# Kernel optimization log

Hardware: AMD Instinct MI355X
Metric: run time of the kernel (lower is better)

Reference implementation:

```python
import jax, jax.numpy as jnp
import numpy as np

B_, L, DM = 2, 1024, 1024
D_STATE, D_CONV, EXPAND = 16, 4, 2
DI = EXPAND * DM          # 2048 inner dim
DTR = DM // 16            # 64 dt rank


def setup_inputs() -> dict:
    key = jax.random.key(0)
    ks = jax.random.split(key, 16)
    g = lambda k, shp, s: jax.random.normal(k, shp, jnp.float32) * s
    inp = {
        "x": g(ks[0], (B_, L, DM), 1.0),
        "ln_g": jnp.ones((DM,), jnp.float32),
        "ln_b": jnp.zeros((DM,), jnp.float32),
        "in_proj_w": g(ks[1], (2 * DI, DM), (2.0 / (DM + 2 * DI)) ** 0.5),
        "conv_w": g(ks[2], (DI, 1, D_CONV), (2.0 / D_CONV) ** 0.5),
        "conv_b": jnp.zeros((DI,), jnp.float32),
        "dtin_w": g(ks[3], (DTR, DI), (2.0 / (DI + DTR)) ** 0.5),
        "dtin_b": jnp.zeros((DTR,), jnp.float32),
        "dt_w": g(ks[4], (DI, DTR), DTR ** -0.5),
        "dt_b": jnp.log(jnp.expm1(jax.random.uniform(ks[5], (DI,), jnp.float32, 1e-3, 0.1))),  # inverse-softplus of dt in [dt_min, dt_max]
        "B_w": g(ks[6], (D_STATE, DI), DI ** -0.5),
        "C_w": g(ks[7], (D_STATE, DI), DI ** -0.5),
        "A_log": jnp.log(jnp.broadcast_to(jnp.arange(1, D_STATE + 1, dtype=jnp.float32), (DI, D_STATE))),
        "D": jnp.ones((DI,), jnp.float32),
        "out_w": g(ks[8], (DM, DI), (2.0 / (DM + DI)) ** 0.5),
    }
    return inp


def _layernorm(x, g, b, eps=1e-5):
    mu = jnp.mean(x, -1, keepdims=True)
    var = jnp.mean(jnp.square(x - mu), -1, keepdims=True)
    return (x - mu) * jax.lax.rsqrt(var + eps) * g + b


def _selective_scan(u, dt, Bm, Cm, A, Dp):
    # u,dt: (b,l,di); Bm,Cm: (b,l,n); A: (di,n)
    def step(h, inp):
        dt_t, B_t, C_t, u_t = inp  # (b,di),(b,n),(b,n),(b,di)
        dA = jnp.exp(dt_t[..., None] * A)                       # (b,di,n)
        h = h * dA + (dt_t * u_t)[..., None] * B_t[:, None, :]   # (b,di,n)
        y = jnp.einsum("bdn,bn->bd", h, C_t)
        return h, y

    tm = lambda a: jnp.swapaxes(a, 0, 1)  # time-major
    h0 = jnp.zeros((u.shape[0], u.shape[2], A.shape[1]), u.dtype)
    _, ys = jax.lax.scan(step, h0, (tm(dt), tm(Bm), tm(Cm), tm(u)))
    return jnp.swapaxes(ys, 0, 1) + u * Dp  # (b,l,di)


def reference(x, ln_g, ln_b, in_proj_w, conv_w, conv_b, dtin_w, dtin_b,
              dt_w, dt_b, B_w, C_w, A_log, D, out_w):
    residual = x
    xn = _layernorm(x, ln_g, ln_b)
    xz = xn @ in_proj_w.T                       # (b,l,2*di)
    x_proj, z = jnp.split(xz, 2, axis=-1)
    # causal depthwise conv1d (left pad d_conv-1, truncate to seq_len)
    xp = jnp.pad(x_proj, ((0, 0), (D_CONV - 1, 0), (0, 0)))
    x_conv = conv_b
    for k in range(D_CONV):
        x_conv = x_conv + conv_w[:, 0, k] * xp[:, k:k + L, :]
    x_conv = jax.nn.silu(x_conv)
    dt_in = x_conv @ dtin_w.T + dtin_b          # (b,l,dtr)
    dt = jax.nn.softplus(dt_in @ dt_w.T + dt_b) # (b,l,di)
    Bm = x_conv @ B_w.T                         # (b,l,n)
    Cm = x_conv @ C_w.T
    A = -jnp.exp(A_log)                         # (di,n)
    y = _selective_scan(x_conv, dt, Bm, Cm, A, D)
    y = y * jax.nn.silu(z)
    return y @ out_w.T + residual
```

## Files before the change

### kernel.cpp

```cpp
#include <hip/hip_runtime.h>
#include <hip/hip_bf16.h>
#include <cstdint>

#define BL    2
#define LSEQ  1024
#define DMOD  1024
#define DIN   2048
#define NST   16
#define DTRK  64
#define MR    (BL*LSEQ)

#define CCH 32
#define TCH 32
#define KSPLIT 8

typedef __bf16 bf16x8 __attribute__((ext_vector_type(8)));
typedef float  f32x4  __attribute__((ext_vector_type(4)));

#if __has_builtin(__builtin_amdgcn_exp2f)
#define EXP2F(x) __builtin_amdgcn_exp2f(x)
#else
#define EXP2F(x) exp2f(x)
#endif
#define LOG2E 1.4426950408889634f

__device__ __forceinline__ void glds16(const void* g, const void* l) {
    __builtin_amdgcn_global_load_lds(
        (__attribute__((address_space(1))) void*)(uintptr_t)(g),
        (__attribute__((address_space(3))) void*)(uint32_t)(uintptr_t)(l),
        16, 0, 0);
}

template <int MODE, int TM, int TN>
__global__ __launch_bounds__(256, 4) void gemm_bt(
    const __hip_bfloat16* __restrict__ A, int lda,
    const __hip_bfloat16* __restrict__ Bw, int ldb,
    int M, int N, int Ksl,
    void* __restrict__ e0, void* __restrict__ e1,
    const float* __restrict__ bias)
{
    constexpr int WM = TM / 2, WN = TN / 2;
    constexpr int MT = WM / 16, NT = WN / 16;
    constexpr int NDA = TM / 64, NDB = TN / 64;
    __shared__ __align__(16) __hip_bfloat16 sA[2][TM * 32];
    __shared__ __align__(16) __hip_bfloat16 sB[2][TN * 32];

    int bx = blockIdx.x, by = blockIdx.y;
    if ((gridDim.y & 7) == 0) {
        const int bid = blockIdx.x + gridDim.x * blockIdx.y;
        const int xcd = bid & 7, s = bid >> 3;
        bx = s % gridDim.x;
        by = (s / gridDim.x) * 8 + xcd;
    }
    const int m0 = by * TM;
    const int n0 = bx * TN;
    const int k0 = blockIdx.z * Ksl;
    const int tid = threadIdx.x;
    const int w = tid >> 6, lane = tid & 63;
    const int wm = (w >> 1) * WM, wn = (w & 1) * WN;
    const int lrow = lane & 15, lq = lane >> 4;

    const int r0 = tid >> 2;
    const int qs = ((tid & 3) - (r0 >> 1)) & 3;
    const __hip_bfloat16* pa[NDA];
    const __hip_bfloat16* pb[NDB];
#pragma unroll
    for (int i = 0; i < NDA; i++) pa[i] = A + (size_t)(m0 + r0 + 64 * i) * lda + k0 + qs * 8;
#pragma unroll
    for (int i = 0; i < NDB; i++) pb[i] = Bw + (size_t)(n0 + r0 + 64 * i) * ldb + k0 + qs * 8;

    f32x4 acc[MT][NT];
#pragma unroll
    for (int i = 0; i < MT; i++)
#pragma unroll
        for (int j = 0; j < NT; j++) { acc[i][j][0]=0.f; acc[i][j][1]=0.f; acc[i][j][2]=0.f; acc[i][j][3]=0.f; }

    const int nk = Ksl >> 5;
#pragma unroll
    for (int i = 0; i < NDA; i++) glds16(pa[i], &sA[0][i * 2048 + tid * 8]);
#pragma unroll
    for (int i = 0; i < NDB; i++) glds16(pb[i], &sB[0][i * 2048 + tid * 8]);

    for (int kb = 0; kb < nk; ++kb) {
        const int cur = kb & 1, nxt = cur ^ 1;
        __syncthreads();
        if (kb + 1 < nk) {
#pragma unroll
            for (int i = 0; i < NDA; i++) { pa[i] += 32; glds16(pa[i], &sA[nxt][i * 2048 + tid * 8]); }
#pragma unroll
            for (int i = 0; i < NDB; i++) { pb[i] += 32; glds16(pb[i], &sB[nxt][i * 2048 + tid * 8]); }
        }
        bf16x8 af[MT], bb[NT];
#pragma unroll
        for (int mt = 0; mt < MT; mt++) {
            const int row = wm + mt * 16 + lrow;
            af[mt] = *(const bf16x8*)&sA[cur][row * 32 + (((lq + (row >> 1)) & 3) * 8)];
        }
#pragma unroll
        for (int nt = 0; nt < NT; nt++) {
            const int row = wn + nt * 16 + lrow;
            bb[nt] = *(const bf16x8*)&sB[cur][row * 32 + (((lq + (row >> 1)) & 3) * 8)];
        }
#pragma unroll
        for (int mt = 0; mt < MT; mt++)
#pragma unroll
            for (int nt = 0; nt < NT; nt++)
                acc[mt][nt] = __builtin_amdgcn_mfma_f32_16x16x32_bf16(af[mt], bb[nt], acc[mt][nt], 0, 0, 0);
    }

#pragma unroll
    for (int mt = 0; mt < MT; mt++) {
#pragma unroll
        for (int nt = 0; nt < NT; nt++) {
            const int gn = n0 + wn + nt * 16 + lrow;
            if (gn >= N) continue;
            const int gmb = m0 + wm + mt * 16 + lq * 4;
#pragma unroll
            for (int r = 0; r < 4; r++) {
                const int gm = gmb + r;
                const float v = acc[mt][nt][r];
                if (MODE == 0) {
                    if (gn < DIN) ((__hip_bfloat16*)e0)[(size_t)gm * DIN + gn] = __float2bfloat16(v);
                    else {
                        const float s = v / (1.f + __expf(-v));
                        ((__hip_bfloat16*)e1)[(size_t)gm * DIN + (gn - DIN)] = __float2bfloat16(s);
                    }
                } else if (MODE == 1) {
                    ((float*)e0)[((size_t)blockIdx.z * M + gm) * 96 + gn] = v;
                } else if (MODE == 2) {
                    const float xx = v + bias[gn];
                    ((float*)e0)[(size_t)gm * N + gn] = (xx > 20.f) ? xx : log1pf(__expf(xx));
                } else {
                    ((float*)e0)[(size_t)gm * N + gn] = v + ((const float*)e1)[(size_t)gm * N + gn];
                }
            }
        }
    }
}

__global__ void ep1_kernel(const float* __restrict__ part, const float* __restrict__ dtin_b,
                           __hip_bfloat16* __restrict__ dtinb, float* __restrict__ Bmf,
                           float* __restrict__ Cmf) {
    const int i = blockIdx.x * 256 + threadIdx.x;
    if (i >= MR * 96) return;
    const int m = i / 96, n = i - m * 96;
    float s = 0.f;
#pragma unroll
    for (int z = 0; z < KSPLIT; z++) s += part[((size_t)z * MR + m) * 96 + n];
    if (n < 64)      dtinb[(size_t)m * 64 + n] = __float2bfloat16(s + dtin_b[n]);
    else if (n < 80) Bmf[(size_t)m * NST + (n - 64)] = s;
    else             Cmf[(size_t)m * NST + (n - 80)] = s;
}

__global__ void cvt_all(const float* __restrict__ w_in, const float* __restrict__ dtin_w,
                        const float* __restrict__ B_w, const float* __restrict__ C_w,
                        const float* __restrict__ dt_w, const float* __restrict__ out_w,
                        __hip_bfloat16* __restrict__ w1b, __hip_bfloat16* __restrict__ wpb,
                        __hip_bfloat16* __restrict__ dtwb, __hip_bfloat16* __restrict__ owb) {
    const int NV = (4194304 + 131072 + 32768 + 32768 + 131072 + 2097152) / 4;
    for (int v = blockIdx.x * 256 + threadIdx.x; v < NV; v += gridDim.x * 256) {
        const int i = v * 4;
        const float* s; __hip_bfloat16* dk;
        if      (i < 4194304) { s = w_in   + i;             dk = w1b  + i; }
        else if (i < 4325376) { s = dtin_w + (i - 4194304); dk = wpb  + (i - 4194304); }
        else if (i < 4358144) { s = B_w    + (i - 4325376); dk = wpb  + 131072 + (i - 4325376); }
        else if (i < 4390912) { s = C_w    + (i - 4358144); dk = wpb  + 163840 + (i - 4358144); }
        else if (i < 4521984) { s = dt_w   + (i - 4390912); dk = dtwb + (i - 4390912); }
        else                  { s = out_w  + (i - 4521984); dk = owb  + (i - 4521984); }
        const float4 f = *(const float4*)s;
        __hip_bfloat16 t0 = __float2bfloat16(f.x), t1 = __float2bfloat16(f.y);
        __hip_bfloat16 t2 = __float2bfloat16(f.z), t3 = __float2bfloat16(f.w);
        ushort4 o;
        o.x = *(unsigned short*)&t0; o.y = *(unsigned short*)&t1;
        o.z = *(unsigned short*)&t2; o.w = *(unsigned short*)&t3;
        *(ushort4*)dk = o;
    }
}

__global__ void ln_kernel(const float* __restrict__ x, const float* __restrict__ g,
                          const float* __restrict__ b, __hip_bfloat16* __restrict__ xn) {
    const int row = blockIdx.x;
    const int tid = threadIdx.x;
    const float4 v = ((const float4*)(x + (size_t)row * DMOD))[tid];
    float s  = v.x + v.y + v.z + v.w;
    float sq = v.x * v.x + v.y * v.y + v.z * v.z + v.w * v.w;
#pragma unroll
    for (int off = 32; off >= 1; off >>= 1) {
        s  += __shfl_down(s, off, 64);
        sq += __shfl_down(sq, off, 64);
    }
    __shared__ float red[8];
    const int w = tid >> 6, lane = tid & 63;
    if (lane == 0) { red[w] = s; red[4 + w] = sq; }
    __syncthreads();
    s  = red[0] + red[1] + red[2] + red[3];
    sq = red[4] + red[5] + red[6] + red[7];
    const float mean = s * (1.f / DMOD);
    const float rstd = rsqrtf(sq * (1.f / DMOD) - mean * mean + 1e-5f);
    const int col = tid * 4;
    const float vv[4] = {v.x, v.y, v.z, v.w};
#pragma unroll
    for (int i = 0; i < 4; i++)
        xn[(size_t)row * DMOD + col + i] =
            __float2bfloat16((vv[i] - mean) * rstd * g[col + i] + b[col + i]);
}

__global__ void conv_silu_kernel(const __hip_bfloat16* __restrict__ xp, const float* __restrict__ cw,
                                 const float* __restrict__ cb,
                                 __hip_bfloat16* __restrict__ xcb) {
    const int d = blockIdx.x * 256 + threadIdx.x;
    const int m0 = blockIdx.y * 64;
    const int l0 = m0 & (LSEQ - 1);
    const float w0 = cw[d * 4], w1 = cw[d * 4 + 1], w2 = cw[d * 4 + 2], w3 = cw[d * 4 + 3];
    const float cbd = cb[d];
    float x0 = 0.f, x1 = 0.f, x2 = 0.f;
    if (l0 != 0) {
        x0 = __bfloat162float(xp[(size_t)(m0 - 3) * DIN + d]);
        x1 = __bfloat162float(xp[(size_t)(m0 - 2) * DIN + d]);
        x2 = __bfloat162float(xp[(size_t)(m0 - 1) * DIN + d]);
    }
#pragma unroll 4
    for (int i = 0; i < 64; i++) {
        const float x3 = __bfloat162float(xp[(size_t)(m0 + i) * DIN + d]);
        const float a = cbd + w0 * x0 + w1 * x1 + w2 * x2 + w3 * x3;
        const float sv = a / (1.f + __expf(-a));
        xcb[(size_t)(m0 + i) * DIN + d] = __float2bfloat16(sv);
        x0 = x1; x1 = x2; x2 = x3;
    }
}


__global__ __launch_bounds__(256) void scan_p1(
    const float* __restrict__ dt, const __hip_bfloat16* __restrict__ u,
    const float* __restrict__ Bm, const float* __restrict__ A_log,
    float* __restrict__ Aprod, float* __restrict__ Bacc)
{
    __shared__ float sB[TCH * NST];
    const int blk = blockIdx.x;
    const int bb = blk >> 9, c = (blk >> 4) & 31, dtile = blk & 15;
    const int tid = threadIdx.x;
    const int nh = tid & 1, dl = tid >> 1;
    const int d = dtile * 128 + dl;
    const int row0 = bb * LSEQ + c * TCH;

    sB[tid]       = Bm[(size_t)row0 * NST + tid];
    sB[tid + 256] = Bm[(size_t)row0 * NST + tid + 256];
    __syncthreads();

    float a2[8];
    {
        const float4 al0 = *(const float4*)&A_log[(size_t)d * NST + nh * 8];
        const float4 al1 = *(const float4*)&A_log[(size_t)d * NST + nh * 8 + 4];
        a2[0] = -__expf(al0.x) * LOG2E; a2[1] = -__expf(al0.y) * LOG2E;
        a2[2] = -__expf(al0.z) * LOG2E; a2[3] = -__expf(al0.w) * LOG2E;
        a2[4] = -__expf(al1.x) * LOG2E; a2[5] = -__expf(al1.y) * LOG2E;
        a2[6] = -__expf(al1.z) * LOG2E; a2[7] = -__expf(al1.w) * LOG2E;
    }
    const float* pdt = dt + (size_t)row0 * DIN + d;
    const __hip_bfloat16* pu = u + (size_t)row0 * DIN + d;
    float h[8], Ap[8];
#pragma unroll
    for (int j = 0; j < 8; j++) { h[j] = 0.f; Ap[j] = 1.f; }

#pragma unroll 4
    for (int t = 0; t < TCH; t++) {
        const float dtv = pdt[t * DIN];
        const float uv  = __bfloat162float(pu[t * DIN]);
        const float du = dtv * uv;
        float bv[8];
        *(float4*)&bv[0] = *(const float4*)&sB[t * NST + nh * 8];
        *(float4*)&bv[4] = *(const float4*)&sB[t * NST + nh * 8 + 4];
#pragma unroll
        for (int j = 0; j < 8; j++) {
            const float e = EXP2F(dtv * a2[j]);
            Ap[j] *= e;
            h[j] = h[j] * e + du * bv[j];
        }
    }
    const size_t idx = (((size_t)bb * CCH + c) * DIN + d) * NST + nh * 8;
    *(float4*)&Aprod[idx]     = make_float4(Ap[0], Ap[1], Ap[2], Ap[3]);
    *(float4*)&Aprod[idx + 4] = make_float4(Ap[4], Ap[5], Ap[6], Ap[7]);
    *(float4*)&Bacc[idx]      = make_float4(h[0], h[1], h[2], h[3]);
    *(float4*)&Bacc[idx + 4]  = make_float4(h[4], h[5], h[6], h[7]);
}

__global__ __launch_bounds__(256) void scan_p2(
    const float* __restrict__ Aprod, const float* __restrict__ Bacc,
    float* __restrict__ hstart)
{
    const int i = blockIdx.x * 256 + threadIdx.x;
    const int bb = i >> 15;
    const int dn = i & 32767;
    float hs = 0.f;
#pragma unroll
    for (int c = 0; c < CCH; c++) {
        const size_t idx = (((size_t)bb * CCH + c) << 15) + dn;
        hstart[idx] = hs;
        hs = Aprod[idx] * hs + Bacc[idx];
    }
}

__global__ __launch_bounds__(256) void scan_p3(
    const float* __restrict__ dt, const __hip_bfloat16* __restrict__ u,
    const float* __restrict__ Bm, const float* __restrict__ Cm,
    const float* __restrict__ A_log, const float* __restrict__ Dp,
    const __hip_bfloat16* __restrict__ zs, const float* __restrict__ hstart,
    __hip_bfloat16* __restrict__ y)
{
    __shared__ float sB[TCH * NST], sC[TCH * NST];
    const int blk = blockIdx.x;
    const int bb = blk >> 9, c = (blk >> 4) & 31, dtile = blk & 15;
    const int tid = threadIdx.x;
    const int nh = tid & 1, dl = tid >> 1;
    const int d = dtile * 128 + dl;
    const int row0 = bb * LSEQ + c * TCH;

    sB[tid]       = Bm[(size_t)row0 * NST + tid];
    sB[tid + 256] = Bm[(size_t)row0 * NST + tid + 256];
    sC[tid]       = Cm[(size_t)row0 * NST + tid];
    sC[tid + 256] = Cm[(size_t)row0 * NST + tid + 256];
    __syncthreads();

    float a2[8];
    {
        const float4 al0 = *(const float4*)&A_log[(size_t)d * NST + nh * 8];
        const float4 al1 = *(const float4*)&A_log[(size_t)d * NST + nh * 8 + 4];
        a2[0] = -__expf(al0.x) * LOG2E; a2[1] = -__expf(al0.y) * LOG2E;
        a2[2] = -__expf(al0.z) * LOG2E; a2[3] = -__expf(al0.w) * LOG2E;
        a2[4] = -__expf(al1.x) * LOG2E; a2[5] = -__expf(al1.y) * LOG2E;
        a2[6] = -__expf(al1.z) * LOG2E; a2[7] = -__expf(al1.w) * LOG2E;
    }
    const float Dd = Dp[d];
    const size_t idx = (((size_t)bb * CCH + c) * DIN + d) * NST + nh * 8;
    float h[8];
    *(float4*)&h[0] = *(const float4*)&hstart[idx];
    *(float4*)&h[4] = *(const float4*)&hstart[idx + 4];

    const float* pdt = dt + (size_t)row0 * DIN + d;
    const __hip_bfloat16* pu = u + (size_t)row0 * DIN + d;
    const __hip_bfloat16* pz = zs + (size_t)row0 * DIN + d;
    __hip_bfloat16* py = y + (size_t)row0 * DIN + d;

#pragma unroll 2
    for (int t = 0; t < TCH; t++) {
        const float dtv = pdt[t * DIN];
        const float uv  = __bfloat162float(pu[t * DIN]);
        const float du = dtv * uv;
        float bv[8], cv[8];
        *(float4*)&bv[0] = *(const float4*)&sB[t * NST + nh * 8];
        *(float4*)&bv[4] = *(const float4*)&sB[t * NST + nh * 8 + 4];
        *(float4*)&cv[0] = *(const float4*)&sC[t * NST + nh * 8];
        *(float4*)&cv[4] = *(const float4*)&sC[t * NST + nh * 8 + 4];
        float yp = 0.f;
#pragma unroll
        for (int j = 0; j < 8; j++) {
            const float e = EXP2F(dtv * a2[j]);
            h[j] = h[j] * e + du * bv[j];
            yp += h[j] * cv[j];
        }
        yp += __shfl_xor(yp, 1, 64);
        if (nh == 0) {
            const float zv = __bfloat162float(pz[t * DIN]);
            py[t * DIN] = __float2bfloat16((yp + uv * Dd) * zv);
        }
    }
}

extern "C" void kernel_launch(void* const* d_in, const int* in_sizes, int n_in,
                              void* d_out, int out_size, void* d_ws, size_t ws_size,
                              hipStream_t stream) {
    const float* x      = (const float*)d_in[0];
    const float* ln_g   = (const float*)d_in[1];
    const float* ln_b   = (const float*)d_in[2];
    const float* w_in   = (const float*)d_in[3];
    const float* conv_w = (const float*)d_in[4];
    const float* conv_b = (const float*)d_in[5];
    const float* dtin_w = (const float*)d_in[6];
    const float* dtin_b = (const float*)d_in[7];
    const float* dt_w   = (const float*)d_in[8];
    const float* dt_b   = (const float*)d_in[9];
    const float* B_w    = (const float*)d_in[10];
    const float* C_w    = (const float*)d_in[11];
    const float* A_log  = (const float*)d_in[12];
    const float* Dp     = (const float*)d_in[13];
    const float* out_w  = (const float*)d_in[14];
    float* out = (float*)d_out;

    char* ws = (char*)d_ws;
    auto alloc = [&](size_t bytes) { char* p = ws; ws += (bytes + 255) & ~255ull; return p; };
    __hip_bfloat16* w1b   = (__hip_bfloat16*)alloc((size_t)4096 * 1024 * 2);
    __hip_bfloat16* wpb   = (__hip_bfloat16*)alloc((size_t)96 * 2048 * 2);
    __hip_bfloat16* dtwb  = (__hip_bfloat16*)alloc((size_t)2048 * 64 * 2);
    __hip_bfloat16* owb   = (__hip_bfloat16*)alloc((size_t)1024 * 2048 * 2);
    __hip_bfloat16* xnb   = (__hip_bfloat16*)alloc((size_t)MR * DMOD * 2);
    __hip_bfloat16* xprojb= (__hip_bfloat16*)alloc((size_t)MR * DIN * 2);
    __hip_bfloat16* zs    = (__hip_bfloat16*)alloc((size_t)MR * DIN * 2);
    __hip_bfloat16* xcb   = (__hip_bfloat16*)alloc((size_t)MR * DIN * 2);
    __hip_bfloat16* dtinb = (__hip_bfloat16*)alloc((size_t)MR * 64 * 2);
    float*          Bmf   = (float*)alloc((size_t)MR * NST * 4);
    float*          Cmf   = (float*)alloc((size_t)MR * NST * 4);
    float*          dtf   = (float*)alloc((size_t)MR * DIN * 4);
    __hip_bfloat16* yb    = (__hip_bfloat16*)alloc((size_t)MR * DIN * 2);
    float*          Aprod = (float*)alloc((size_t)BL * CCH * DIN * NST * 4);
    float*          Bacc  = (float*)alloc((size_t)BL * CCH * DIN * NST * 4);
    float*          hstart= (float*)alloc((size_t)BL * CCH * DIN * NST * 4);
    float*          part  = (float*)w1b;

    cvt_all<<<1024, 256, 0, stream>>>(w_in, dtin_w, B_w, C_w, dt_w, out_w, w1b, wpb, dtwb, owb);
    ln_kernel<<<MR, 256, 0, stream>>>(x, ln_g, ln_b, xnb);

    gemm_bt<0, 64, 128><<<dim3(32, 32, 1), 256, 0, stream>>>(xnb, 1024, w1b, 1024, MR, 4096, 1024,
                                                             xprojb, zs, nullptr);
    conv_silu_kernel<<<dim3(8, 32), 256, 0, stream>>>(xprojb, conv_w, conv_b, xcb);

    gemm_bt<1, 64, 128><<<dim3(1, 32, KSPLIT), 256, 0, stream>>>(xcb, 2048, wpb, 2048, MR, 96, 2048 / KSPLIT,
                                                                 part, nullptr, nullptr);
    ep1_kernel<<<(MR * 96 + 255) / 256, 256, 0, stream>>>(part, dtin_b, dtinb, Bmf, Cmf);

    gemm_bt<2, 64, 128><<<dim3(16, 32, 1), 256, 0, stream>>>(dtinb, 64, dtwb, 64, MR, DIN, 64,
                                                             dtf, nullptr, dt_b);

    scan_p1<<<BL * CCH * 16, 256, 0, stream>>>(dtf, xcb, Bmf, A_log, Aprod, Bacc);
    scan_p2<<<BL * DIN * NST / 256, 256, 0, stream>>>(Aprod, Bacc, hstart);
    scan_p3<<<BL * CCH * 16, 256, 0, stream>>>(dtf, xcb, Bmf, Cmf, A_log, Dp, zs, hstart, yb);

    gemm_bt<3, 64, 64><<<dim3(16, 32, 1), 256, 0, stream>>>(yb, 2048, owb, 2048, MR, DMOD, 2048,
                                                            out, (void*)x, nullptr);
}
```

Baseline: 253.9 us.

## Fuse prep kernels, use atomic split-K, bf16 dt, and merge scan phases

Merges weight conversion, layernorm, zeroing of accumulators, and the residual copy into one prep kernel. The x_proj GEMM now reduces its split-K partials with atomics, which removes the epilogue kernel. The dt GEMM adds the bias and converts to bf16 while staging its A tile, and writes dt as bf16 to halve scan traffic. Scan phases 1 and 2 are merged using a last-block counter, and the out-projection uses 128x128 tiles with 4-way split-K atomics onto the prefilled residual. In exchange it adds atomic contention, nondeterministic summation order, and reduced dt precision.

Measured after the change: 415.3 us. 63.6% more time.

```diff
diff --git a/kernel.cpp b/kernel.cpp
--- a/kernel.cpp
+++ b/kernel.cpp
@@ -12,7 +12,6 @@
 
 #define CCH 32
 #define TCH 32
-#define KSPLIT 8
 
 typedef __bf16 bf16x8 __attribute__((ext_vector_type(8)));
 typedef float  f32x4  __attribute__((ext_vector_type(4)));
@@ -31,13 +30,35 @@
         16, 0, 0);
 }
 
+__device__ __forceinline__ __bf16 f2b(float f) {
+    __hip_bfloat16 t = __float2bfloat16(f);
+    return *(__bf16*)&t;
+}
+
+__device__ __forceinline__ void stage_dtin(const float* __restrict__ Af,
+                                           const float* __restrict__ bias,
+                                           __hip_bfloat16* dst, int m0, int r0,
+                                           int qs, int kb) {
+    const int col0 = kb * 32 + qs * 8;
+    const float4 f0 = *(const float4*)&Af[(size_t)(m0 + r0) * 64 + col0];
+    const float4 f1 = *(const float4*)&Af[(size_t)(m0 + r0) * 64 + col0 + 4];
+    const float4 b0 = *(const float4*)&bias[col0];
+    const float4 b1 = *(const float4*)&bias[col0 + 4];
+    bf16x8 o;
+    o[0] = f2b(f0.x + b0.x); o[1] = f2b(f0.y + b0.y);
+    o[2] = f2b(f0.z + b0.z); o[3] = f2b(f0.w + b0.w);
+    o[4] = f2b(f1.x + b1.x); o[5] = f2b(f1.y + b1.y);
+    o[6] = f2b(f1.z + b1.z); o[7] = f2b(f1.w + b1.w);
+    *(bf16x8*)dst = o;
+}
+
 template <int MODE, int TM, int TN>
-__global__ __launch_bounds__(256, 4) void gemm_bt(
+__global__ __launch_bounds__(256, (TM * TN <= 8192) ? 4 : 2) void gemm_bt(
     const __hip_bfloat16* __restrict__ A, int lda,
     const __hip_bfloat16* __restrict__ Bw, int ldb,
     int M, int N, int Ksl,
-    void* __restrict__ e0, void* __restrict__ e1,
-    const float* __restrict__ bias)
+    void* __restrict__ e0, void* __restrict__ e1, void* __restrict__ e2,
+    const float* __restrict__ bias, const float* __restrict__ Af)
 {
     constexpr int WM = TM / 2, WN = TN / 2;
     constexpr int MT = WM / 16, NT = WN / 16;
@@ -64,8 +85,10 @@
     const int qs = ((tid & 3) - (r0 >> 1)) & 3;
     const __hip_bfloat16* pa[NDA];
     const __hip_bfloat16* pb[NDB];
-#pragma unroll
-    for (int i = 0; i < NDA; i++) pa[i] = A + (size_t)(m0 + r0 + 64 * i) * lda + k0 + qs * 8;
+    if constexpr (MODE != 2) {
+#pragma unroll
+        for (int i = 0; i < NDA; i++) pa[i] = A + (size_t)(m0 + r0 + 64 * i) * lda + k0 + qs * 8;
+    }
 #pragma unroll
     for (int i = 0; i < NDB; i++) pb[i] = Bw + (size_t)(n0 + r0 + 64 * i) * ldb + k0 + qs * 8;
 
@@ -76,8 +99,12 @@
         for (int j = 0; j < NT; j++) { acc[i][j][0]=0.f; acc[i][j][1]=0.f; acc[i][j][2]=0.f; acc[i][j][3]=0.f; }
 
     const int nk = Ksl >> 5;
-#pragma unroll
-    for (int i = 0; i < NDA; i++) glds16(pa[i], &sA[0][i * 2048 + tid * 8]);
+    if constexpr (MODE == 2) {
+        stage_dtin(Af, bias, &sA[0][tid * 8], m0, r0, qs, 0);
+    } else {
+#pragma unroll
+        for (int i = 0; i < NDA; i++) glds16(pa[i], &sA[0][i * 2048 + tid * 8]);
+    }
 #pragma unroll
     for (int i = 0; i < NDB; i++) glds16(pb[i], &sB[0][i * 2048 + tid * 8]);
 
@@ -85,8 +112,12 @@
         const int cur = kb & 1, nxt = cur ^ 1;
         __syncthreads();
         if (kb + 1 < nk) {
-#pragma unroll
-            for (int i = 0; i < NDA; i++) { pa[i] += 32; glds16(pa[i], &sA[nxt][i * 2048 + tid * 8]); }
+            if constexpr (MODE == 2) {
+                stage_dtin(Af, bias, &sA[nxt][tid * 8], m0, r0, qs, kb + 1);
+            } else {
+#pragma unroll
+                for (int i = 0; i < NDA; i++) { pa[i] += 32; glds16(pa[i], &sA[nxt][i * 2048 + tid * 8]); }
+            }
 #pragma unroll
             for (int i = 0; i < NDB; i++) { pb[i] += 32; glds16(pb[i], &sB[nxt][i * 2048 + tid * 8]); }
         }
@@ -126,83 +157,87 @@
                         ((__hip_bfloat16*)e1)[(size_t)gm * DIN + (gn - DIN)] = __float2bfloat16(s);
                     }
                 } else if (MODE == 1) {
-                    ((float*)e0)[((size_t)blockIdx.z * M + gm) * 96 + gn] = v;
+                    if (gn < 64)      atomicAdd((float*)e0 + (size_t)gm * 64 + gn, v);
+                    else if (gn < 80) atomicAdd((float*)e1 + (size_t)gm * NST + (gn - 64), v);
+                    else              atomicAdd((float*)e2 + (size_t)gm * NST + (gn - 80), v);
                 } else if (MODE == 2) {
-                    const float xx = v + bias[gn];
-                    ((float*)e0)[(size_t)gm * N + gn] = (xx > 20.f) ? xx : log1pf(__expf(xx));
+                    const float xx = v + ((const float*)e1)[gn];
+                    const float sp = (xx > 20.f) ? xx : log1pf(__expf(xx));
+                    ((__hip_bfloat16*)e0)[(size_t)gm * N + gn] = __float2bfloat16(sp);
                 } else {
-                    ((float*)e0)[(size_t)gm * N + gn] = v + ((const float*)e1)[(size_t)gm * N + gn];
+                    atomicAdd((float*)e0 + (size_t)gm * N + gn, v);
                 }
             }
         }
     }
 }
 
-__global__ void ep1_kernel(const float* __restrict__ part, const float* __restrict__ dtin_b,
-                           __hip_bfloat16* __restrict__ dtinb, float* __restrict__ Bmf,
-                           float* __restrict__ Cmf) {
-    const int i = blockIdx.x * 256 + threadIdx.x;
-    if (i >= MR * 96) return;
-    const int m = i / 96, n = i - m * 96;
-    float s = 0.f;
-#pragma unroll
-    for (int z = 0; z < KSPLIT; z++) s += part[((size_t)z * MR + m) * 96 + n];
-    if (n < 64)      dtinb[(size_t)m * 64 + n] = __float2bfloat16(s + dtin_b[n]);
-    else if (n < 80) Bmf[(size_t)m * NST + (n - 64)] = s;
-    else             Cmf[(size_t)m * NST + (n - 80)] = s;
-}
-
-__global__ void cvt_all(const float* __restrict__ w_in, const float* __restrict__ dtin_w,
-                        const float* __restrict__ B_w, const float* __restrict__ C_w,
-                        const float* __restrict__ dt_w, const float* __restrict__ out_w,
-                        __hip_bfloat16* __restrict__ w1b, __hip_bfloat16* __restrict__ wpb,
-                        __hip_bfloat16* __restrict__ dtwb, __hip_bfloat16* __restrict__ owb) {
-    const int NV = (4194304 + 131072 + 32768 + 32768 + 131072 + 2097152) / 4;
-    for (int v = blockIdx.x * 256 + threadIdx.x; v < NV; v += gridDim.x * 256) {
-        const int i = v * 4;
-        const float* s; __hip_bfloat16* dk;
-        if      (i < 4194304) { s = w_in   + i;             dk = w1b  + i; }
-        else if (i < 4325376) { s = dtin_w + (i - 4194304); dk = wpb  + (i - 4194304); }
-        else if (i < 4358144) { s = B_w    + (i - 4325376); dk = wpb  + 131072 + (i - 4325376); }
-        else if (i < 4390912) { s = C_w    + (i - 4358144); dk = wpb  + 163840 + (i - 4358144); }
-        else if (i < 4521984) { s = dt_w   + (i - 4390912); dk = dtwb + (i - 4390912); }
-        else                  { s = out_w  + (i - 4521984); dk = owb  + (i - 4521984); }
-        const float4 f = *(const float4*)s;
-        __hip_bfloat16 t0 = __float2bfloat16(f.x), t1 = __float2bfloat16(f.y);
-        __hip_bfloat16 t2 = __float2bfloat16(f.z), t3 = __float2bfloat16(f.w);
-        ushort4 o;
-        o.x = *(unsigned short*)&t0; o.y = *(unsigned short*)&t1;
-        o.z = *(unsigned short*)&t2; o.w = *(unsigned short*)&t3;
-        *(ushort4*)dk = o;
-    }
-}
-
-__global__ void ln_kernel(const float* __restrict__ x, const float* __restrict__ g,
-                          const float* __restrict__ b, __hip_bfloat16* __restrict__ xn) {
-    const int row = blockIdx.x;
+#define NCVT 1654784
+#define NZRO 49160
+#define NCPY 524288
+__global__ void prep_kernel(const float* __restrict__ x, const float* __restrict__ ln_g,
+                            const float* __restrict__ ln_b,
+                            const float* __restrict__ w_in, const float* __restrict__ dtin_w,
+                            const float* __restrict__ B_w, const float* __restrict__ C_w,
+                            const float* __restrict__ dt_w, const float* __restrict__ out_w,
+                            __hip_bfloat16* __restrict__ w1b, __hip_bfloat16* __restrict__ wpb,
+                            __hip_bfloat16* __restrict__ dtwb, __hip_bfloat16* __restrict__ owb,
+                            __hip_bfloat16* __restrict__ xn, float* __restrict__ zblock,
+                            float* __restrict__ out)
+{
+    const int b = blockIdx.x;
     const int tid = threadIdx.x;
-    const float4 v = ((const float4*)(x + (size_t)row * DMOD))[tid];
-    float s  = v.x + v.y + v.z + v.w;
-    float sq = v.x * v.x + v.y * v.y + v.z * v.z + v.w * v.w;
-#pragma unroll
-    for (int off = 32; off >= 1; off >>= 1) {
-        s  += __shfl_down(s, off, 64);
-        sq += __shfl_down(sq, off, 64);
-    }
-    __shared__ float red[8];
-    const int w = tid >> 6, lane = tid & 63;
-    if (lane == 0) { red[w] = s; red[4 + w] = sq; }
-    __syncthreads();
-    s  = red[0] + red[1] + red[2] + red[3];
-    sq = red[4] + red[5] + red[6] + red[7];
-    const float mean = s * (1.f / DMOD);
-    const float rstd = rsqrtf(sq * (1.f / DMOD) - mean * mean + 1e-5f);
-    const int col = tid * 4;
-    const float vv[4] = {v.x, v.y, v.z, v.w};
-#pragma unroll
-    for (int i = 0; i < 4; i++)
-        xn[(size_t)row * DMOD + col + i] =
-            __float2bfloat16((vv[i] - mean) * rstd * g[col + i] + b[col + i]);
+    if (b < MR) {
+        const float4 v = ((const float4*)(x + (size_t)b * DMOD))[tid];
+        float s  = v.x + v.y + v.z + v.w;
+        float sq = v.x * v.x + v.y * v.y + v.z * v.z + v.w * v.w;
+#pragma unroll
+        for (int off = 32; off >= 1; off >>= 1) {
+            s  += __shfl_down(s, off, 64);
+            sq += __shfl_down(sq, off, 64);
+        }
+        __shared__ float red[8];
+        const int w = tid >> 6, lane = tid & 63;
+        if (lane == 0) { red[w] = s; red[4 + w] = sq; }
+        __syncthreads();
+        s  = red[0] + red[1] + red[2] + red[3];
+        sq = red[4] + red[5] + red[6] + red[7];
+        const float mean = s * (1.f / DMOD);
+        const float rstd = rsqrtf(sq * (1.f / DMOD) - mean * mean + 1e-5f);
+        const int col = tid * 4;
+        const float vv[4] = {v.x, v.y, v.z, v.w};
+#pragma unroll
+        for (int i = 0; i < 4; i++)
+            xn[(size_t)b * DMOD + col + i] =
+                __float2bfloat16((vv[i] - mean) * rstd * ln_g[col + i] + ln_b[col + i]);
+        return;
+    }
+    const int nb = gridDim.x - MR;
+    for (int v4 = (b - MR) * 256 + tid; v4 < NCVT + NZRO + NCPY; v4 += nb * 256) {
+        if (v4 < NCVT) {
+            const int i = v4 * 4;
+            const float* s; __hip_bfloat16* dk;
+            if      (i < 4194304) { s = w_in   + i;             dk = w1b  + i; }
+            else if (i < 4325376) { s = dtin_w + (i - 4194304); dk = wpb  + (i - 4194304); }
+            else if (i < 4358144) { s = B_w    + (i - 4325376); dk = wpb  + 131072 + (i - 4325376); }
+            else if (i < 4390912) { s = C_w    + (i - 4358144); dk = wpb  + 163840 + (i - 4358144); }
+            else if (i < 4521984) { s = dt_w   + (i - 4390912); dk = dtwb + (i - 4390912); }
+            else                  { s = out_w  + (i - 4521984); dk = owb  + (i - 4521984); }
+            const float4 f = *(const float4*)s;
+            bf16x8 dummy; (void)dummy;
+            ushort4 o;
+            o.x = (unsigned short)(__hip_bfloat16_raw(__float2bfloat16(f.x)).x);
+            o.y = (unsigned short)(__hip_bfloat16_raw(__float2bfloat16(f.y)).x);
+            o.z = (unsigned short)(__hip_bfloat16_raw(__float2bfloat16(f.z)).x);
+            o.w = (unsigned short)(__hip_bfloat16_raw(__float2bfloat16(f.w)).x);
+            *(ushort4*)dk = o;
+        } else if (v4 < NCVT + NZRO) {
+            float4 z; z.x = z.y = z.z = z.w = 0.f;
+            ((float4*)zblock)[v4 - NCVT] = z;
+        } else {
+            ((float4*)out)[v4 - NCVT - NZRO] = ((const float4*)x)[v4 - NCVT - NZRO];
+        }
+    }
 }
 
 __global__ void conv_silu_kernel(const __hip_bfloat16* __restrict__ xp, const float* __restrict__ cw,
@@ -229,13 +264,14 @@
     }
 }
 
-
-__global__ __launch_bounds__(256) void scan_p1(
-    const float* __restrict__ dt, const __hip_bfloat16* __restrict__ u,
+__global__ __launch_bounds__(256) void scan_p12(
+    const __hip_bfloat16* __restrict__ dt, const __hip_bfloat16* __restrict__ u,
     const float* __restrict__ Bm, const float* __restrict__ A_log,
-    float* __restrict__ Aprod, float* __restrict__ Bacc)
+    float* __restrict__ Aprod, float* __restrict__ Bacc,
+    float* __restrict__ hstart, int* __restrict__ cnt)
 {
     __shared__ float sB[TCH * NST];
+    __shared__ int lastFlag;
     const int blk = blockIdx.x;
     const int bb = blk >> 9, c = (blk >> 4) & 31, dtile = blk & 15;
     const int tid = threadIdx.x;
@@ -256,15 +292,15 @@
         a2[4] = -__expf(al1.x) * LOG2E; a2[5] = -__expf(al1.y) * LOG2E;
         a2[6] = -__expf(al1.z) * LOG2E; a2[7] = -__expf(al1.w) * LOG2E;
     }
-    const float* pdt = dt + (size_t)row0 * DIN + d;
-    const __hip_bfloat16* pu = u + (size_t)row0 * DIN + d;
+    const __hip_bfloat16* pdt = dt + (size_t)row0 * DIN + d;
+    const __hip_bfloat16* pu  = u  + (size_t)row0 * DIN + d;
     float h[8], Ap[8];
 #pragma unroll
     for (int j = 0; j < 8; j++) { h[j] = 0.f; Ap[j] = 1.f; }
 
 #pragma unroll 4
     for (int t = 0; t < TCH; t++) {
-        const float dtv = pdt[t * DIN];
+        const float dtv = __bfloat162float(pdt[t * DIN]);
         const float uv  = __bfloat162float(pu[t * DIN]);
         const float du = dtv * uv;
         float bv[8];
@@ -282,26 +318,37 @@
     *(float4*)&Aprod[idx + 4] = make_float4(Ap[4], Ap[5], Ap[6], Ap[7]);
     *(float4*)&Bacc[idx]      = make_float4(h[0], h[1], h[2], h[3]);
     *(float4*)&Bacc[idx + 4]  = make_float4(h[4], h[5], h[6], h[7]);
-}
-
-__global__ __launch_bounds__(256) void scan_p2(
-    const float* __restrict__ Aprod, const float* __restrict__ Bacc,
-    float* __restrict__ hstart)
-{
-    const int i = blockIdx.x * 256 + threadIdx.x;
-    const int bb = i >> 15;
-    const int dn = i & 32767;
-    float hs = 0.f;
-#pragma unroll
-    for (int c = 0; c < CCH; c++) {
-        const size_t idx = (((size_t)bb * CCH + c) << 15) + dn;
-        hstart[idx] = hs;
-        hs = Aprod[idx] * hs + Bacc[idx];
+
+    __threadfence();
+    __syncthreads();
+    if (tid == 0) {
+        const int g = bb * 16 + dtile;
+        lastFlag = (atomicAdd(&cnt[g], 1) == CCH - 1);
+    }
+    __syncthreads();
+    if (!lastFlag) return;
+    __threadfence();
+    const int dd = dtile * 128 + (tid >> 1);
+    const int n0 = (tid & 1) * 8;
+    float4 hs0 = make_float4(0.f, 0.f, 0.f, 0.f);
+    float4 hs1 = make_float4(0.f, 0.f, 0.f, 0.f);
+    for (int cc = 0; cc < CCH; cc++) {
+        const size_t base = (((size_t)bb * CCH + cc) * DIN + dd) * NST + n0;
+        *(float4*)&hstart[base]     = hs0;
+        *(float4*)&hstart[base + 4] = hs1;
+        const float4 ap0 = *(const float4*)&Aprod[base];
+        const float4 ap1 = *(const float4*)&Aprod[base + 4];
+        const float4 bc0 = *(const float4*)&Bacc[base];
+        const float4 bc1 = *(const float4*)&Bacc[base + 4];
+        hs0.x = ap0.x * hs0.x + bc0.x; hs0.y = ap0.y * hs0.y + bc0.y;
+        hs0.z = ap0.z * hs0.z + bc0.z; hs0.w = ap0.w * hs0.w + bc0.w;
+        hs1.x = ap1.x * hs1.x + bc1.x; hs1.y = ap1.y * hs1.y + bc1.y;
+        hs1.z = ap1.z * hs1.z + bc1.z; hs1.w = ap1.w * hs1.w + bc1.w;
     }
 }
 
 __global__ __launch_bounds__(256) void scan_p3(
-    const float* __restrict__ dt, const __hip_bfloat16* __restrict__ u,
+    const __hip_bfloat16* __restrict__ dt, const __hip_bfloat16* __restrict__ u,
     const float* __restrict__ Bm, const float* __restrict__ Cm,
     const float* __restrict__ A_log, const float* __restrict__ Dp,
     const __hip_bfloat16* __restrict__ zs, const float* __restrict__ hstart,
@@ -336,14 +383,14 @@
     *(float4*)&h[0] = *(const float4*)&hstart[idx];
     *(float4*)&h[4] = *(const float4*)&hstart[idx + 4];
 
-    const float* pdt = dt + (size_t)row0 * DIN + d;
-    const __hip_bfloat16* pu = u + (size_t)row0 * DIN + d;
-    const __hip_bfloat16* pz = zs + (size_t)row0 * DIN + d;
+    const __hip_bfloat16* pdt = dt + (size_t)row0 * DIN + d;
+    const __hip_bfloat16* pu  = u  + (size_t)row0 * DIN + d;
+    const __hip_bfloat16* pz  = zs + (size_t)row0 * DIN + d;
     __hip_bfloat16* py = y + (size_t)row0 * DIN + d;
 
 #pragma unroll 2
     for (int t = 0; t < TCH; t++) {
-        const float dtv = pdt[t * DIN];
+        const float dtv = __bfloat162float(pdt[t * DIN]);
         const float uv  = __bfloat162float(pu[t * DIN]);
         const float du = dtv * uv;
         float bv[8], cv[8];
@@ -396,34 +443,35 @@
     __hip_bfloat16* xprojb= (__hip_bfloat16*)alloc((size_t)MR * DIN * 2);
     __hip_bfloat16* zs    = (__hip_bfloat16*)alloc((size_t)MR * DIN * 2);
     __hip_bfloat16* xcb   = (__hip_bfloat16*)alloc((size_t)MR * DIN * 2);
-    __hip_bfloat16* dtinb = (__hip_bfloat16*)alloc((size_t)MR * 64 * 2);
-    float*          Bmf   = (float*)alloc((size_t)MR * NST * 4);
-    float*          Cmf   = (float*)alloc((size_t)MR * NST * 4);
-    float*          dtf   = (float*)alloc((size_t)MR * DIN * 4);
+    __hip_bfloat16* dtb   = (__hip_bfloat16*)alloc((size_t)MR * DIN * 2);
     __hip_bfloat16* yb    = (__hip_bfloat16*)alloc((size_t)MR * DIN * 2);
+    float*          zblock= (float*)alloc((size_t)(196608 + 32) * 4);
     float*          Aprod = (float*)alloc((size_t)BL * CCH * DIN * NST * 4);
     float*          Bacc  = (float*)alloc((size_t)BL * CCH * DIN * NST * 4);
     float*          hstart= (float*)alloc((size_t)BL * CCH * DIN * NST * 4);
-    float*          part  = (float*)w1b;
-
-    cvt_all<<<1024, 256, 0, stream>>>(w_in, dtin_w, B_w, C_w, dt_w, out_w, w1b, wpb, dtwb, owb);
-    ln_kernel<<<MR, 256, 0, stream>>>(x, ln_g, ln_b, xnb);
-
-    gemm_bt<0, 64, 128><<<dim3(32, 32, 1), 256, 0, stream>>>(xnb, 1024, w1b, 1024, MR, 4096, 1024,
-                                                             xprojb, zs, nullptr);
+
+    float* fdtin = zblock;
+    float* Bmf   = zblock + 131072;
+    float* Cmf   = zblock + 163840;
+    int*   cnt   = (int*)(zblock + 196608);
+
+    prep_kernel<<<MR + 896, 256, 0, stream>>>(x, ln_g, ln_b, w_in, dtin_w, B_w, C_w, dt_w,
+                                              out_w, w1b, wpb, dtwb, owb, xnb, zblock, out);
+
+    gemm_bt<0, 64, 128><<<dim3(32, 32, 1), 256, 0, stream>>>(
+        xnb, 1024, w1b, 1024, MR, 4096, 1024, xprojb, zs, nullptr, nullptr, nullptr);
+
     conv_silu_kernel<<<dim3(8, 32), 256, 0, stream>>>(xprojb, conv_w, conv_b, xcb);
 
-    gemm_bt<1, 64, 128><<<dim3(1, 32, KSPLIT), 256, 0, stream>>>(xcb, 2048, wpb, 2048, MR, 96, 2048 / KSPLIT,
-                                                                 part, nullptr, nullptr);
-    ep1_kernel<<<(MR * 96 + 255) / 256, 256, 0, stream>>>(part, dtin_b, dtinb, Bmf, Cmf);
-
-    gemm_bt<2, 64, 128><<<dim3(16, 32, 1), 256, 0, stream>>>(dtinb, 64, dtwb, 64, MR, DIN, 64,
-                                                             dtf, nullptr, dt_b);
-
-    scan_p1<<<BL * CCH * 16, 256, 0, stream>>>(dtf, xcb, Bmf, A_log, Aprod, Bacc);
-    scan_p2<<<BL * DIN * NST / 256, 256, 0, stream>>>(Aprod, Bacc, hstart);
-    scan_p3<<<BL * CCH * 16, 256, 0, stream>>>(dtf, xcb, Bmf, Cmf, A_log, Dp, zs, hstart, yb);
-
-    gemm_bt<3, 64, 64><<<dim3(16, 32, 1), 256, 0, stream>>>(yb, 2048, owb, 2048, MR, DMOD, 2048,
-                                                            out, (void*)x, nullptr);
-}
+    gemm_bt<1, 64, 128><<<dim3(1, 32, 8), 256, 0, stream>>>(
+        xcb, 2048, wpb, 2048, MR, 96, 256, fdtin, Bmf, Cmf, nullptr, nullptr);
+
+    gemm_bt<2, 64, 128><<<dim3(16, 32, 1), 256, 0, stream>>>(
+        nullptr, 0, dtwb, 64, MR, DIN, 64, dtb, (void*)dt_b, nullptr, dtin_b, fdtin);
+
+    scan_p12<<<BL * CCH * 16, 256, 0, stream>>>(dtb, xcb, Bmf, A_log, Aprod, Bacc, hstart, cnt);
+    scan_p3<<<BL * CCH * 16, 256, 0, stream>>>(dtb, xcb, Bmf, Cmf, A_log, Dp, zs, hstart, yb);
+
+    gemm_bt<3, 128, 128><<<dim3(8, 16, 4), 256, 0, stream>>>(
+        yb, 2048, owb, 2048, MR, DMOD, 512, out, nullptr, nullptr, nullptr, nullptr);
+}
```
